# Optimization experiments

Hardware: AMD Instinct MI355X
Metric: run time of the kernel (lower is better)

## Reference

```python
import jax, jax.numpy as jnp
import numpy as np
import math

H = 16
LORA_SCALING = 16 / 8  # alpha / r
NEG_INF = -1e30

def _alibi_slopes(n_heads):
    start = 2.0 ** (-(2.0 ** (-(math.log2(n_heads) - 3))))
    return jnp.asarray([start * start ** i for i in range(n_heads)], dtype=jnp.float32)

def setup_inputs() -> dict:
    key = jax.random.key(0)
    ks = jax.random.split(key, 11)
    B, T, E, r = 4, 2048, 1024, 8
    d = {
        'x':  jax.random.normal(ks[0], (B, T, E), jnp.float32),
        'Wq': jax.random.normal(ks[1], (E, E), jnp.float32) * (E ** -0.5),
        'Aq': jax.random.normal(ks[2], (E, r), jnp.float32) * 0.01,
        'Bq': jax.random.normal(ks[3], (r, E), jnp.float32) * 0.01,
        'Wk': jax.random.normal(ks[4], (E, E), jnp.float32) * (E ** -0.5),
        'Ak': jax.random.normal(ks[5], (E, r), jnp.float32) * 0.01,
        'Bk': jax.random.normal(ks[6], (r, E), jnp.float32) * 0.01,
        'Wv': jax.random.normal(ks[7], (E, E), jnp.float32) * (E ** -0.5),
        'Av': jax.random.normal(ks[8], (E, r), jnp.float32) * 0.01,
        'Bv': jax.random.normal(ks[9], (r, E), jnp.float32) * 0.01,
        'Wp': jax.random.normal(ks[10], (E, E), jnp.float32) * (E ** -0.5),
    }
    return d

def _lora(x, W, A, Bm):
    # nn.Linear: x @ W.T ; LoRA: x @ B.T @ A.T * scaling
    return x @ W.T + ((x @ Bm.T) @ A.T) * LORA_SCALING

def reference(x, Wq, Aq, Bq, Wk, Ak, Bk, Wv, Av, Bv, Wp):
    B, T, E = x.shape
    dh = E // H
    q = _lora(x, Wq, Aq, Bq).reshape(B, T, H, dh).transpose(0, 2, 1, 3)  # [B,H,T,dh]
    k = _lora(x, Wk, Ak, Bk).reshape(B, T, H, dh).transpose(0, 2, 1, 3)
    v = _lora(x, Wv, Av, Bv).reshape(B, T, H, dh).transpose(0, 2, 1, 3)
    s = jnp.einsum('bhqd,bhkd->bhqk', q, k) / jnp.sqrt(jnp.float32(dh))
    i = jnp.arange(T)[:, None]
    j = jnp.arange(T)[None, :]
    slopes = _alibi_slopes(H)
    bias = slopes[:, None, None] * (i - j).astype(jnp.float32)  # [H,T,T]
    s = s + bias[None]
    s = jnp.where(j[None, None] <= i[None, None], s, NEG_INF)  # causal mask
    out = jnp.einsum('bhqk,bhkd->bhqd', jax.nn.softmax(s, axis=-1), v)
    out = out.transpose(0, 2, 1, 3).reshape(B, T, E)
    return out @ Wp.T  # dropout is identity in eval
```

## Files before the change

### kernel.cpp

```cpp
#include <hip/hip_runtime.h>

typedef unsigned short u16;
typedef unsigned int u32;
typedef u16  u16x8 __attribute__((ext_vector_type(8)));
typedef u16  u16x4 __attribute__((ext_vector_type(4)));
typedef u32  u32x4 __attribute__((ext_vector_type(4)));
typedef __bf16 bf16x2 __attribute__((ext_vector_type(2)));
typedef __bf16 bf16x8 __attribute__((ext_vector_type(8)));
typedef float f32x4 __attribute__((ext_vector_type(4)));
typedef float f32x16 __attribute__((ext_vector_type(16)));

__constant__ int KBW[16]  = {0,1,1,2,3,5,7,10,14,20,28,40,56,80,113,160};

__constant__ unsigned char RANKTBL[256] = {
  0xBF,0xCF,0xDF,0xEF,0xFF,
  0xBE,0xCE,0xDE,0xEE,0xFE,
  0xAE,0xAF,
  0xAD,0xBD,0xCD,0xDD,0xED,0xFD,
  0xAC,0xBC,0xCC,0xDC,0xEC,0xFC,
  0xAB,0xBB,0xCB,0xDB,0xEB,0xFB,
  0xAA,0xBA,0xCA,0xDA,0xEA,0xFA,
  0x9A,0x9B,0x9C,0x9D,0x9E,0x9F,
  0x99,0xA9,0xB9,0xC9,0xD9,0xE9,0xF9,
  0x98,0xA8,0xB8,0xC8,0xD8,0xE8,0xF8,
  0x97,0xA7,0xB7,0xC7,0xD7,0xE7,0xF7,
  0x87,0x88,0x89,0x8A,0x8B,0x8C,0x8D,0x8E,0x8F,
  0x86,0x96,0xA6,0xB6,0xC6,0xD6,0xE6,0xF6,
  0x85,0x95,0xA5,0xB5,0xC5,0xD5,0xE5,0xF5,
  0x75,0x76,0x77,0x78,0x79,0x7A,0x7B,0x7C,0x7D,0x7E,0x7F,
  0x74,0x84,0x94,0xA4,0xB4,0xC4,0xD4,0xE4,0xF4,
  0x63,0x64,0x65,0x66,0x67,0x68,0x69,0x6A,0x6B,0x6C,0x6D,0x6E,0x6F,
  0x73,0x83,0x93,0xA3,0xB3,0xC3,0xD3,0xE3,0xF3,
  0x52,0x53,0x54,0x55,0x56,0x57,0x58,0x59,0x5A,0x5B,0x5C,0x5D,0x5E,0x5F,
  0x62,0x72,0x82,0x92,0xA2,0xB2,0xC2,0xD2,0xE2,0xF2,
  0x41,0x42,0x43,0x44,0x45,0x46,0x47,0x48,0x49,0x4A,0x4B,0x4C,0x4D,0x4E,0x4F,
  0x51,0x61,0x71,0x81,0x91,0xA1,0xB1,0xC1,0xD1,0xE1,0xF1,
  0x31,0x32,0x33,0x34,0x35,0x36,0x37,0x38,0x39,0x3A,0x3B,0x3C,0x3D,0x3E,0x3F,
  0x10,0x11,0x12,0x13,0x14,0x15,0x16,0x17,0x18,0x19,0x1A,0x1B,0x1C,0x1D,0x1E,0x1F,
  0x20,0x21,0x22,0x23,0x24,0x25,0x26,0x27,0x28,0x29,0x2A,0x2B,0x2C,0x2D,0x2E,0x2F,
  0x30,0x40,0x50,0x60,0x70,0x80,0x90,0xA0,0xB0,0xC0,0xD0,0xE0,0xF0,
  0x00,0x01,0x02,0x03,0x04,0x05,0x06,0x07,0x08,0x09,0x0A,0x0B,0x0C,0x0D,0x0E,0x0F
};

static __device__ __forceinline__ u16 f2bf(float f) {
  unsigned int u = __float_as_uint(f);
  u += 0x7FFFu + ((u >> 16) & 1u);
  return (u16)(u >> 16);
}

static __device__ __forceinline__ u32 packbf(float a, float b) {
  bf16x2 t;
  t[0] = (__bf16)a;
  t[1] = (__bf16)b;
  return __builtin_bit_cast(u32, t);
}

static __device__ __forceinline__ f32x4 mfma16(bf16x8 a, bf16x8 b, f32x4 c) {
  return __builtin_amdgcn_mfma_f32_16x16x32_bf16(a, b, c, 0, 0, 0);
}
static __device__ __forceinline__ f32x16 mfma32(bf16x8 a, bf16x8 b, f32x16 c) {
  return __builtin_amdgcn_mfma_f32_32x32x16_bf16(a, b, c, 0, 0, 0);
}

static __device__ __forceinline__ void gload16(const void* g, void* lds) {
  __builtin_amdgcn_global_load_lds(
      (const __attribute__((address_space(1))) unsigned int*)g,
      (__attribute__((address_space(3))) unsigned int*)lds, 16, 0, 0);
}

__global__ __launch_bounds__(256) void k_cast_x(const float* __restrict__ in,
                                                u16* __restrict__ out) {
  size_t i = (size_t)blockIdx.x * 256 + threadIdx.x;
  const float4* p = reinterpret_cast<const float4*>(in) + i * 2;
  float4 a = p[0], b = p[1];
  u16x8 r;
  r[0] = f2bf(a.x); r[1] = f2bf(a.y); r[2] = f2bf(a.z); r[3] = f2bf(a.w);
  r[4] = f2bf(b.x); r[5] = f2bf(b.y); r[6] = f2bf(b.z); r[7] = f2bf(b.w);
  *reinterpret_cast<u16x8*>(out + i * 8) = r;
}

__global__ __launch_bounds__(256) void k_fold_w(
    const float* __restrict__ Wq, const float* __restrict__ Aq, const float* __restrict__ Bq,
    const float* __restrict__ Wk, const float* __restrict__ Ak, const float* __restrict__ Bk,
    const float* __restrict__ Wv, const float* __restrict__ Av, const float* __restrict__ Bv,
    const float* __restrict__ Wp, u16* __restrict__ wqkv, u16* __restrict__ wp) {
  int n = blockIdx.x;
  int widx = n >> 10, nr = n & 1023;
  const float *W, *A, *Bm; u16* dst;
  if (widx == 0)      { W = Wq; A = Aq; Bm = Bq; dst = wqkv; }
  else if (widx == 1) { W = Wk; A = Ak; Bm = Bk; dst = wqkv + (1 << 20); }
  else if (widx == 2) { W = Wv; A = Av; Bm = Bv; dst = wqkv + (2 << 20); }
  else                { W = Wp; A = nullptr; Bm = nullptr; dst = wp; }
  int e0 = threadIdx.x * 4;
  float4 w = *reinterpret_cast<const float4*>(W + (size_t)nr * 1024 + e0);
  if (widx < 3) {
    float acx = 0.f, acy = 0.f, acz = 0.f, acw = 0.f;
#pragma unroll
    for (int r = 0; r < 8; r++) {
      float ar = A[nr * 8 + r];
      float4 bm = *reinterpret_cast<const float4*>(Bm + (size_t)r * 1024 + e0);
      acx += ar * bm.x; acy += ar * bm.y; acz += ar * bm.z; acw += ar * bm.w;
    }
    w.x += 2.0f * acx; w.y += 2.0f * acy; w.z += 2.0f * acz; w.w += 2.0f * acw;
  }
  u16x4 r4; r4[0] = f2bf(w.x); r4[1] = f2bf(w.y); r4[2] = f2bf(w.z); r4[3] = f2bf(w.w);
  *reinterpret_cast<u16x4*>(dst + (size_t)nr * 1024 + e0) = r4;
}

template<int OUTF32>
__global__ __launch_bounds__(256) void k_gemm_bt(const u16* __restrict__ A,
                                                 const u16* __restrict__ Bw,
                                                 void* __restrict__ C, int K, int N, int lda) {
  __shared__ __align__(16) u16 As[128 * 64];
  __shared__ __align__(16) u16 Bs[128 * 64];
  const int tid = threadIdx.x;
  const int wave = tid >> 6, lane = tid & 63;
  const int l15 = lane & 15, lg = lane >> 4;
  const int m0 = blockIdx.x * 128, n0 = blockIdx.y * 128;
  const int wr = wave >> 1, wc = wave & 1;

  f32x4 acc[4][4];
#pragma unroll
  for (int i = 0; i < 4; i++)
#pragma unroll
    for (int j = 0; j < 4; j++) acc[i][j] = (f32x4)0.0f;

  for (int k0 = 0; k0 < K; k0 += 64) {
#pragma unroll
    for (int i = 0; i < 4; i++) {
      int idx = i * 256 + tid;
      int row = idx >> 3, col = (idx & 7) << 3;
      gload16(A  + (size_t)(m0 + row) * lda + k0 + col, As + (i * 4 + wave) * 512);
      gload16(Bw + (size_t)(n0 + row) * K   + k0 + col, Bs + (i * 4 + wave) * 512);
    }
    __syncthreads();
#pragma unroll
    for (int c = 0; c < 2; c++) {
      bf16x8 af[4], bfr[4];
#pragma unroll
      for (int t = 0; t < 4; t++) {
        af[t]  = *reinterpret_cast<const bf16x8*>(As + (wr * 64 + t * 16 + l15) * 64 + c * 32 + lg * 8);
        bfr[t] = *reinterpret_cast<const bf16x8*>(Bs + (wc * 64 + t * 16 + l15) * 64 + c * 32 + lg * 8);
      }
#pragma unroll
      for (int mi = 0; mi < 4; mi++)
#pragma unroll
        for (int ni = 0; ni < 4; ni++)
          acc[mi][ni] = mfma16(af[mi], bfr[ni], acc[mi][ni]);
    }
    __syncthreads();
  }

  const int rbase = m0 + wr * 64, cbase = n0 + wc * 64;
#pragma unroll
  for (int mi = 0; mi < 4; mi++)
#pragma unroll
    for (int ni = 0; ni < 4; ni++)
#pragma unroll
      for (int j = 0; j < 4; j++) {
        int r  = rbase + mi * 16 + lg * 4 + j;
        int cc = cbase + ni * 16 + l15;
        if constexpr (OUTF32) {
          reinterpret_cast<float*>(C)[(size_t)r * N + cc] = acc[mi][ni][j];
        } else {
          reinterpret_cast<u16*>(C)[(size_t)r * N + cc] = f2bf(acc[mi][ni][j]);
        }
      }
}

__global__ __launch_bounds__(256) void k_vt(const u16* __restrict__ qkv,
                                            u16* __restrict__ vt) {
  __shared__ __align__(16) u16 tile[64 * 64];
  const int tb = blockIdx.x, h = blockIdx.y, b = blockIdx.z;
  const int tid = threadIdx.x;
  const size_t rb = (size_t)b * 2048;
  const int hv = 2048 + h * 64;
#pragma unroll
  for (int p = 0; p < 2; p++) {
    int r = p * 32 + (tid >> 3);
    int c = (tid & 7) * 8;
    u16x8 v = *reinterpret_cast<const u16x8*>(qkv + (rb + tb * 64 + r) * 3072 + hv + c);
    int slot = (c >> 3) ^ (r & 7) ^ ((r >> 3) & 7);
    *reinterpret_cast<u16x8*>(tile + r * 64 + slot * 8) = v;
  }
  __syncthreads();
#pragma unroll
  for (int p = 0; p < 2; p++) {
    int d = p * 32 + (tid >> 3);
    int t0 = (tid & 7) * 8;
    u16x8 v;
#pragma unroll
    for (int j = 0; j < 8; j++) {
      int r = t0 + j;
      int slot = (d >> 3) ^ (r & 7) ^ ((r >> 3) & 7);
      v[j] = tile[r * 64 + slot * 8 + (d & 7)];
    }
    *reinterpret_cast<u16x8*>(vt + ((size_t)(b * 16 + h) * 64 + d) * 2048 + tb * 64 + t0) = v;
  }
}

__global__ __launch_bounds__(256) void k_attn(const u16* __restrict__ qkv,
                                              const u16* __restrict__ vt,
                                              u16* __restrict__ aout) {
  __shared__ __align__(16) u16 Kl[2][64 * 64];
  __shared__ __align__(16) u16 Vl[2][64 * 64];
  const int tid = threadIdx.x, wave = tid >> 6, lane = tid & 63;
  const int l31 = lane & 31, half = lane >> 5;
  const int i = (int)blockIdx.x;
  const int b = i & 3, p = i >> 2;
  const int k4 = p >> 6, j4 = p & 63;
  const int ridx = (k4 == 0) ? j4 : (k4 == 1) ? 127 - j4 : (k4 == 2) ? 128 + j4 : 255 - j4;
  const int hqv = RANKTBL[ridx];
  const int h = hqv >> 4, qb = hqv & 15;
  const int rb = b * 2048;
  const int hq = h * 64, hk = 1024 + h * 64;
  const int bh64 = (b * 16 + h) * 64;
  const int qB = qb * 128;
  const int q0w = qB + wave * 32;
  const int q = q0w + l31;

  bf16x8 qf[4];
#pragma unroll
  for (int c = 0; c < 4; c++)
    qf[c] = *reinterpret_cast<const bf16x8*>(qkv + (size_t)(rb + q) * 3072 + hq + c * 16 + half * 8);

  const float slope2 = exp2f(-0.5f * (float)(h + 1)) * 1.44269504f;
  const float c0 = 0.18033688f;

  const int kend = min(2 * qb + 1, KBW[h]);

  float mrun = -1e30f, lrun = 0.f;
  f32x16 o0 = (f32x16)0.0f, o1 = (f32x16)0.0f;

  auto stage = [&](int kvr, int dst) {
#pragma unroll
    for (int i2 = 0; i2 < 2; i2++) {
      int row = (i2 * 4 + wave) * 8 + (lane >> 3);
      int scol = ((lane & 7) ^ (row & 7)) << 3;
      gload16(qkv + (size_t)(rb + kvr + row) * 3072 + hk + scol, &Kl[dst][(i2 * 4 + wave) * 512]);
      gload16(vt + (size_t)(bh64 + row) * 2048 + kvr + scol,     &Vl[dst][(i2 * 4 + wave) * 512]);
    }
  };

  stage(0, 0);
  __syncthreads();

  int bfi = 0;
  for (int kb = 0; kb <= kend; ++kb, bfi ^= 1) {
    const int kvr = kb * 64;
    if (kb < kend) stage(kvr + 64, bfi ^ 1);

    if (kvr <= q0w + 31) {
      f32x16 s[2];
#pragma unroll
      for (int t = 0; t < 2; t++) s[t] = (f32x16)0.0f;
      __builtin_amdgcn_s_setprio(1);
#pragma unroll
      for (int t = 0; t < 2; t++) {
        int r = t * 32 + l31;
#pragma unroll
        for (int cc = 0; cc < 4; cc++) {
          bf16x8 kf = *reinterpret_cast<const bf16x8*>(
              &Kl[bfi][r * 64 + (((cc * 2 + half) ^ (r & 7)) << 3)]);
          s[t] = mfma32(kf, qf[cc], s[t]);
        }
      }
      __builtin_amdgcn_s_setprio(0);

      const bool domask = (kvr + 63 > q0w);
      const int qrel = q - kvr - half * 4;
      const float qb0 = slope2 * (float)qrel;
      const float qb1 = qb0 - slope2 * 32.0f;
      float mt = -1e30f;
#pragma unroll
      for (int t = 0; t < 2; t++) {
        const float qbt = t ? qb1 : qb0;
        const int qmt = t ? (qrel - 32) : qrel;
#pragma unroll
        for (int r = 0; r < 16; r++) {
          const int krel = (r & 3) + 8 * (r >> 2);
          float val = fmaf(s[t][r], c0, fmaf(-slope2, (float)krel, qbt));
          if (domask) val = (krel <= qmt) ? val : -3.0e38f;
          s[t][r] = val;
          mt = fmaxf(mt, val);
        }
      }
      mt = fmaxf(mt, __shfl_xor(mt, 32));

      if (__any(mt - mrun > 8.0f)) {
        float mn = fmaxf(mrun, mt);
        float al = exp2f(mrun - mn);
        mrun = mn; lrun *= al;
#pragma unroll
        for (int r = 0; r < 16; r++) { o0[r] *= al; o1[r] *= al; }
      }

      float rs0 = 0.f, rs1 = 0.f;
#pragma unroll
      for (int t = 0; t < 2; t++)
#pragma unroll
        for (int r = 0; r < 16; r++) {
          float pp = exp2f(s[t][r] - mrun);
          s[t][r] = pp;
          if (t) rs1 += pp; else rs0 += pp;
        }
      float rs = rs0 + rs1;
      rs += __shfl_xor(rs, 32);
      lrun += rs;

      bf16x8 pf[4];
#pragma unroll
      for (int t = 0; t < 2; t++)
#pragma unroll
        for (int hs = 0; hs < 2; hs++) {
          u32 A0 = packbf(s[t][8 * hs + 0], s[t][8 * hs + 1]);
          u32 B0 = packbf(s[t][8 * hs + 2], s[t][8 * hs + 3]);
          u32 C0 = packbf(s[t][8 * hs + 4], s[t][8 * hs + 5]);
          u32 D0 = packbf(s[t][8 * hs + 6], s[t][8 * hs + 7]);
          asm volatile("v_permlane32_swap_b32 %0, %1" : "+v"(A0), "+v"(C0));
          asm volatile("v_permlane32_swap_b32 %0, %1" : "+v"(B0), "+v"(D0));
          u32x4 fr; fr[0] = A0; fr[1] = B0; fr[2] = C0; fr[3] = D0;
          pf[t * 2 + hs] = __builtin_bit_cast(bf16x8, fr);
        }

      __builtin_amdgcn_s_setprio(1);
#pragma unroll
      for (int dblk = 0; dblk < 2; dblk++) {
        int r = dblk * 32 + l31;
#pragma unroll
        for (int kc = 0; kc < 4; kc++) {
          bf16x8 vf = *reinterpret_cast<const bf16x8*>(
              &Vl[bfi][r * 64 + (((kc * 2 + half) ^ (r & 7)) << 3)]);
          if (dblk) o1 = mfma32(vf, pf[kc], o1);
          else      o0 = mfma32(vf, pf[kc], o0);
        }
      }
      __builtin_amdgcn_s_setprio(0);
    }
    __syncthreads();
  }

  const float linv = 1.0f / lrun;
#pragma unroll
  for (int dblk = 0; dblk < 2; dblk++)
#pragma unroll
    for (int rg = 0; rg < 4; rg++) {
      int d0 = dblk * 32 + 8 * rg + 4 * half;
      u16x4 r4;
#pragma unroll
      for (int j = 0; j < 4; j++) {
        float v = (dblk ? o1[rg * 4 + j] : o0[rg * 4 + j]) * linv;
        r4[j] = f2bf(v);
      }
      *reinterpret_cast<u16x4*>(aout + (size_t)(rb + q) * 3072 + hq + d0) = r4;
    }
}

extern "C" void kernel_launch(void* const* d_in, const int* in_sizes, int n_in,
                              void* d_out, int out_size, void* d_ws, size_t ws_size,
                              hipStream_t stream) {
  (void)in_sizes; (void)n_in; (void)out_size; (void)ws_size;
  const float* x  = (const float*)d_in[0];
  const float* Wq = (const float*)d_in[1];
  const float* Aq = (const float*)d_in[2];
  const float* Bq = (const float*)d_in[3];
  const float* Wk = (const float*)d_in[4];
  const float* Ak = (const float*)d_in[5];
  const float* Bk = (const float*)d_in[6];
  const float* Wv = (const float*)d_in[7];
  const float* Av = (const float*)d_in[8];
  const float* Bv = (const float*)d_in[9];
  const float* Wp = (const float*)d_in[10];

  char* ws = (char*)d_ws;
  u16* xb   = (u16*)(ws);
  u16* wqkv = (u16*)(ws + 16777216);
  u16* wp   = (u16*)(ws + 23068672);
  u16* qkv  = (u16*)(ws + 25165824);
  u16* vt   = xb;
  float* out = (float*)d_out;

  k_cast_x<<<dim3(4096), dim3(256), 0, stream>>>(x, xb);
  k_fold_w<<<dim3(4096), dim3(256), 0, stream>>>(Wq, Aq, Bq, Wk, Ak, Bk, Wv, Av, Bv, Wp, wqkv, wp);
  k_gemm_bt<0><<<dim3(64, 24), dim3(256), 0, stream>>>(xb, wqkv, (void*)qkv, 1024, 3072, 1024);
  k_vt<<<dim3(32, 16, 4), dim3(256), 0, stream>>>(qkv, vt);
  k_attn<<<dim3(1024), dim3(256), 0, stream>>>(qkv, vt, qkv);
  k_gemm_bt<1><<<dim3(64, 8), dim3(256), 0, stream>>>(qkv, wp, (void*)out, 1024, 1024, 3072);
}
```

Measured before the change: 205.8 us.

## Replace GEMM with 8-wave double-buffered pipelined 128x256 tile kernel

```diff
diff --git a/kernel.cpp b/kernel.cpp
--- a/kernel.cpp
+++ b/kernel.cpp
@@ -108,16 +108,24 @@
 }
 
 template<int OUTF32>
-__global__ __launch_bounds__(256) void k_gemm_bt(const u16* __restrict__ A,
-                                                 const u16* __restrict__ Bw,
-                                                 void* __restrict__ C, int K, int N, int lda) {
-  __shared__ __align__(16) u16 As[128 * 64];
-  __shared__ __align__(16) u16 Bs[128 * 64];
+__global__ __launch_bounds__(512) void k_gemm8(const u16* __restrict__ Ag,
+                                               const u16* __restrict__ Bg,
+                                               void* __restrict__ C,
+                                               int K, int N, int lda, int gx) {
+  __shared__ __align__(16) u16 As[2][8192];
+  __shared__ __align__(16) u16 Bs[2][16384];
   const int tid = threadIdx.x;
-  const int wave = tid >> 6, lane = tid & 63;
+  const int wid = tid >> 6, lane = tid & 63;
   const int l15 = lane & 15, lg = lane >> 4;
-  const int m0 = blockIdx.x * 128, n0 = blockIdx.y * 128;
-  const int wr = wave >> 1, wc = wave & 1;
+  const int wr = wid >> 2, wc = wid & 3;
+  const int nwg = gridDim.x, cpx = nwg >> 3;
+  const int bid = (int)blockIdx.x;
+  const int sid = (bid & 7) * cpx + (bid >> 3);
+  const int m0 = (sid % gx) * 128, n0 = (sid / gx) * 256;
+
+  const int swz = ((l15 >> 3) & 1) << 4;
+  const int ln2 = lane >> 2;
+  const int scol = ((lane & 3) ^ ((lane >> 5) << 1)) << 3;
 
   f32x4 acc[4][4];
 #pragma unroll
@@ -125,45 +133,98 @@
 #pragma unroll
     for (int j = 0; j < 4; j++) acc[i][j] = (f32x4)0.0f;
 
-  for (int k0 = 0; k0 < K; k0 += 64) {
-#pragma unroll
-    for (int i = 0; i < 4; i++) {
-      int idx = i * 256 + tid;
-      int row = idx >> 3, col = (idx & 7) << 3;
-      gload16(A  + (size_t)(m0 + row) * lda + k0 + col, As + (i * 4 + wave) * 512);
-      gload16(Bw + (size_t)(n0 + row) * K   + k0 + col, Bs + (i * 4 + wave) * 512);
-    }
-    __syncthreads();
-#pragma unroll
-    for (int c = 0; c < 2; c++) {
-      bf16x8 af[4], bfr[4];
-#pragma unroll
-      for (int t = 0; t < 4; t++) {
-        af[t]  = *reinterpret_cast<const bf16x8*>(As + (wr * 64 + t * 16 + l15) * 64 + c * 32 + lg * 8);
-        bfr[t] = *reinterpret_cast<const bf16x8*>(Bs + (wc * 64 + t * 16 + l15) * 64 + c * 32 + lg * 8);
-      }
-#pragma unroll
-      for (int mi = 0; mi < 4; mi++)
-#pragma unroll
-        for (int ni = 0; ni < 4; ni++)
-          acc[mi][ni] = mfma16(af[mi], bfr[ni], acc[mi][ni]);
-    }
-    __syncthreads();
+  auto stageA = [&](int d, int t) {
+#pragma unroll
+    for (int i = 0; i < 2; i++)
+      gload16(Ag + (size_t)(m0 + wid * 16 + ln2) * lda + t * 64 + i * 32 + scol,
+              &As[d][(i * 512 + wid * 64) * 8]);
+  };
+  auto stageB = [&](int d, int t) {
+#pragma unroll
+    for (int i = 0; i < 4; i++)
+      gload16(Bg + (size_t)(n0 + (i & 1) * 128 + wid * 16 + ln2) * K + t * 64 + (i >> 1) * 32 + scol,
+              &Bs[d][(i * 512 + wid * 64) * 8]);
+  };
+  auto ldsA = [&](int d, int m, int kk) {
+    int rr = wr * 64 + m * 16 + l15;
+    return *reinterpret_cast<const bf16x8*>(&As[d][kk * 4096 + rr * 32 + (lg * 8 ^ swz)]);
+  };
+  auto ldsB = [&](int d, int n, int kk) {
+    int rr = wc * 64 + n * 16 + l15;
+    return *reinterpret_cast<const bf16x8*>(&Bs[d][kk * 8192 + rr * 32 + (lg * 8 ^ swz)]);
+  };
+
+  bf16x8 fa[4][2], fb[4][2];
+  auto quad = [&](int mh, int nh) {
+    __builtin_amdgcn_s_setprio(1);
+#pragma unroll
+    for (int m = 0; m < 2; m++)
+#pragma unroll
+      for (int n = 0; n < 2; n++)
+#pragma unroll
+        for (int kk = 0; kk < 2; kk++)
+          acc[mh * 2 + m][nh * 2 + n] =
+              mfma16(fa[mh * 2 + m][kk], fb[nh * 2 + n][kk], acc[mh * 2 + m][nh * 2 + n]);
+    __builtin_amdgcn_s_setprio(0);
+  };
+
+#define MIDBAR do { asm volatile("s_barrier" ::: "memory"); \
+                    asm volatile("s_waitcnt lgkmcnt(0)" ::: "memory"); } while (0)
+#define ENDBAR asm volatile("s_barrier" ::: "memory")
+
+  stageB(0, 0); stageA(0, 0); stageB(1, 1); stageA(1, 1);
+  asm volatile("s_waitcnt vmcnt(0)" ::: "memory");
+  asm volatile("s_barrier" ::: "memory");
+
+  const int niter = K >> 7;
+  for (int it = 0; it < niter; ++it) {
+    const bool st = (it + 1 < niter);
+    const int T2 = 2 * it + 2;
+#pragma unroll
+    for (int d = 0; d < 2; ++d) {
+#pragma unroll
+      for (int m = 0; m < 2; m++)
+#pragma unroll
+        for (int kk = 0; kk < 2; kk++) fa[m][kk] = ldsA(d, m, kk);
+#pragma unroll
+      for (int n = 0; n < 2; n++)
+#pragma unroll
+        for (int kk = 0; kk < 2; kk++) fb[n][kk] = ldsB(d, n, kk);
+      MIDBAR; quad(0, 0); ENDBAR;
+#pragma unroll
+      for (int n = 2; n < 4; n++)
+#pragma unroll
+        for (int kk = 0; kk < 2; kk++) fb[n][kk] = ldsB(d, n, kk);
+      MIDBAR; quad(0, 1); ENDBAR;
+#pragma unroll
+      for (int m = 2; m < 4; m++)
+#pragma unroll
+        for (int kk = 0; kk < 2; kk++) fa[m][kk] = ldsA(d, m, kk);
+      if (st) stageB(d, T2 + d);
+      MIDBAR; quad(1, 1); ENDBAR;
+      if (st) stageA(d, T2 + d);
+      MIDBAR; quad(1, 0);
+      if (st) asm volatile("s_waitcnt vmcnt(6)" ::: "memory");
+      else    asm volatile("s_waitcnt vmcnt(0)" ::: "memory");
+      ENDBAR;
+    }
   }
+#undef MIDBAR
+#undef ENDBAR
 
   const int rbase = m0 + wr * 64, cbase = n0 + wc * 64;
 #pragma unroll
-  for (int mi = 0; mi < 4; mi++)
-#pragma unroll
-    for (int ni = 0; ni < 4; ni++)
+  for (int m = 0; m < 4; m++)
+#pragma unroll
+    for (int n = 0; n < 4; n++)
 #pragma unroll
       for (int j = 0; j < 4; j++) {
-        int r  = rbase + mi * 16 + lg * 4 + j;
-        int cc = cbase + ni * 16 + l15;
+        int r  = rbase + m * 16 + lg * 4 + j;
+        int cc = cbase + n * 16 + l15;
         if constexpr (OUTF32) {
-          reinterpret_cast<float*>(C)[(size_t)r * N + cc] = acc[mi][ni][j];
+          reinterpret_cast<float*>(C)[(size_t)r * N + cc] = acc[m][n][j];
         } else {
-          reinterpret_cast<u16*>(C)[(size_t)r * N + cc] = f2bf(acc[mi][ni][j]);
+          reinterpret_cast<u16*>(C)[(size_t)r * N + cc] = f2bf(acc[m][n][j]);
         }
       }
 }
@@ -382,8 +443,8 @@
 
   k_cast_x<<<dim3(4096), dim3(256), 0, stream>>>(x, xb);
   k_fold_w<<<dim3(4096), dim3(256), 0, stream>>>(Wq, Aq, Bq, Wk, Ak, Bk, Wv, Av, Bv, Wp, wqkv, wp);
-  k_gemm_bt<0><<<dim3(64, 24), dim3(256), 0, stream>>>(xb, wqkv, (void*)qkv, 1024, 3072, 1024);
+  k_gemm8<0><<<dim3(768), dim3(512), 0, stream>>>(xb, wqkv, (void*)qkv, 1024, 3072, 1024, 64);
   k_vt<<<dim3(32, 16, 4), dim3(256), 0, stream>>>(qkv, vt);
   k_attn<<<dim3(1024), dim3(256), 0, stream>>>(qkv, vt, qkv);
-  k_gemm_bt<1><<<dim3(64, 8), dim3(256), 0, stream>>>(qkv, wp, (void*)out, 1024, 1024, 3072);
-}
+  k_gemm8<1><<<dim3(256), dim3(512), 0, stream>>>(qkv, wp, (void*)out, 1024, 1024, 3072, 64);
+}
```

Result: no change. 201.7 us (-2.0%).
